# Kernel optimization log

Hardware: AMD Instinct MI355X
Metric: run time of the kernel (lower is better)

Reference implementation:

```python
import jax, jax.numpy as jnp
import numpy as np
import math

DIM = 384; HEADS = 12; HD = 32; L_REL = 4; L_STD = 12; MLP_H = 4 * DIM
B = 8; N = 256
N_REL = 1
TIME_SCALE = 30000.0 / 500 * 0.3
SCALE = HD ** -0.5
NEG = -1e9  # finite stand-in for -inf padding mask (identical softmax result, safe grads)


def _ln(x, g, b):
    m = x.mean(-1, keepdims=True)
    v = ((x - m) ** 2).mean(-1, keepdims=True)
    return (x - m) / jnp.sqrt(v + 1e-5) * g + b


def _sin_emb(x, dim):
    half = dim // 2
    freq = jnp.exp(jnp.arange(half, dtype=x.dtype) * (-math.log(10000.0) / half))
    e = x[..., None] * freq
    return jnp.concatenate([jnp.sin(e), jnp.cos(e)], -1)


def _rel_bias(x0, w1d, b1d, wp, bp):
    pos = x0[..., :3]
    t = x0[..., 3:4]
    dpos = pos[:, :, None] - pos[:, None, :]                 # [B,N,N,3]
    dt = t[:, :, None] - t[:, None, :] * TIME_SCALE          # [B,N,N,1] (scale on 2nd term, as in torch)
    dpos2 = dpos ** 2
    dt2 = dt ** 2
    ds2 = dpos2.sum(-1) - dt2[..., 0]
    d = jnp.sign(ds2) * jnp.sqrt(jnp.abs(ds2))
    f = jnp.concatenate([dpos, dt, dpos2, dt2], -1)          # [B,N,N,8]
    d = d + (f @ w1d.T + b1d)[..., 0]
    emb = _sin_emb(1024.0 * jnp.clip(d, -4.0, 4.0), HD)      # [B,N,N,HD]
    return emb @ wp.T + bp


def _mask_bias(mask):
    mn = jnp.minimum(mask[:, None, :], mask[:, :, None])
    mx = jnp.maximum(mask[:, None, :], mask[:, :, None])
    return jnp.where(mx < 0, 0.0, mn)                        # [B,N,N]


def _attn(xq, xkv, wq, wk, wv, wo, bo, rel, mbias):
    Bq, Nq, _ = xq.shape
    q = (xq @ wq.T).reshape(Bq, Nq, HEADS, HD).transpose(0, 2, 1, 3) * SCALE
    k = (xkv @ wk.T).reshape(Bq, Nq, HEADS, HD).transpose(0, 2, 1, 3)
    v = (xkv @ wv.T).reshape(Bq, Nq, HEADS, HD).transpose(0, 2, 1, 3)
    a = jnp.einsum('bhic,bhjc->bhij', q, k)
    if rel is not None:
        a = a + jnp.einsum('bhic,bijc->bhij', q, rel)
    if mbias is not None:
        a = a + mbias[:, None]
    a = jax.nn.softmax(a, axis=-1)
    o = jnp.einsum('bhij,bhjc->bihc', a, v)
    if rel is not None:
        o = o + jnp.einsum('bhij,bijc->bihc', a, rel)
    return o.reshape(Bq, Nq, HEADS * HD) @ wo.T + bo


def _mlp(x, w1, b1, w2, b2):
    return jax.nn.gelu(x @ w1.T + b1, approximate=False) @ w2.T + b2


def setup_inputs() -> dict:
    key = jax.random.key(0)
    ks = iter(jax.random.split(key, 64))
    f = lambda shape: jax.random.normal(next(ks), shape, jnp.float32) * 0.02
    inp = {}
    inp['x'] = jax.random.normal(next(ks), (B, N, DIM), jnp.float32)
    inp['x0'] = jax.random.normal(next(ks), (B, N, 4), jnp.float32)
    lengths = jax.random.randint(next(ks), (B,), N // 2, N + 1)
    inp['mask'] = jnp.where(jnp.arange(N)[None, :] < lengths[:, None], 0.0, NEG).astype(jnp.float32)
    inp['rp_w1d'] = f((1, 8)); inp['rp_b1d'] = jnp.zeros((1,), jnp.float32)
    inp['rp_wp'] = f((HD, HD)); inp['rp_bp'] = jnp.zeros((HD,), jnp.float32)
    for p, L in (('sw', L_REL), ('bl', L_STD)):
        inp[p + '_ln1_g'] = jnp.ones((L, DIM), jnp.float32); inp[p + '_ln1_b'] = jnp.zeros((L, DIM), jnp.float32)
        inp[p + '_ln2_g'] = jnp.ones((L, DIM), jnp.float32); inp[p + '_ln2_b'] = jnp.zeros((L, DIM), jnp.float32)
        inp[p + '_wq'] = f((L, DIM, DIM)); inp[p + '_wk'] = f((L, DIM, DIM)); inp[p + '_wv'] = f((L, DIM, DIM))
        inp[p + '_wo'] = f((L, DIM, DIM)); inp[p + '_bo'] = jnp.zeros((L, DIM), jnp.float32)
        inp[p + '_w1'] = f((L, MLP_H, DIM)); inp[p + '_b1'] = jnp.zeros((L, MLP_H), jnp.float32)
        inp[p + '_w2'] = f((L, DIM, MLP_H)); inp[p + '_b2'] = jnp.zeros((L, DIM), jnp.float32)
    inp['bl_g1'] = jnp.ones((L_STD, DIM), jnp.float32)   # init_values=1
    inp['bl_g2'] = jnp.ones((L_STD, DIM), jnp.float32)
    inp['cls_w'] = f((DIM,))
    inp['out_w'] = f((3, DIM)); inp['out_b'] = jnp.zeros((3,), jnp.float32)
    return inp


def reference(x, x0, mask, rp_w1d, rp_b1d, rp_wp, rp_bp,
              sw_ln1_g, sw_ln1_b, sw_ln2_g, sw_ln2_b, sw_wq, sw_wk, sw_wv, sw_wo, sw_bo,
              sw_w1, sw_b1, sw_w2, sw_b2,
              bl_ln1_g, bl_ln1_b, bl_ln2_g, bl_ln2_b, bl_wq, bl_wk, bl_wv, bl_wo, bl_bo,
              bl_w1, bl_b1, bl_w2, bl_b2, bl_g1, bl_g2, cls_w, out_w, out_b):
    rel = _rel_bias(x0, rp_w1d, rp_b1d, rp_wp, rp_bp)
    mbias = _mask_bias(mask)
    for i in range(L_REL):
        r = rel if i < N_REL else None
        xn = _ln(x, sw_ln1_g[i], sw_ln1_b[i])
        x = x + _attn(xn, xn, sw_wq[i], sw_wk[i], sw_wv[i], sw_wo[i], sw_bo[i], r, mbias)
        x = x + _mlp(_ln(x, sw_ln2_g[i], sw_ln2_b[i]), sw_w1[i], sw_b1[i], sw_w2[i], sw_b2[i])
    # prepend cls token; it is always valid
    cls = jnp.broadcast_to(cls_w[None, None, :], (x.shape[0], 1, DIM))
    x = jnp.concatenate([cls, x], axis=1)
    mask2 = jnp.concatenate([jnp.zeros((x.shape[0], 1), mask.dtype), mask], axis=1)
    mbias2 = _mask_bias(mask2)
    for i in range(L_STD):
        xn = _ln(x, bl_ln1_g[i], bl_ln1_b[i])
        x = x + bl_g1[i] * _attn(xn, xn, bl_wq[i], bl_wk[i], bl_wv[i], bl_wo[i], bl_bo[i], None, mbias2)
        x = x + bl_g2[i] * _mlp(_ln(x, bl_ln2_g[i], bl_ln2_b[i]), bl_w1[i], bl_b1[i], bl_w2[i], bl_b2[i])
    return x[:, 0] @ out_w.T + out_b   # [B, 3]
```

## Files before the change

kernel.cpp:

```cpp
#include <hip/hip_runtime.h>
#include <hip/hip_bf16.h>
#include <math.h>

#define DIM 384
#define HEADS 12
#define HD 32
#define MLP_H 1536
#define BATCH 8
#define N1 256
#define N2 257
#define QP 1152
#define SCALE 0.17677669529663687f
#define TIME_SCALE 18.0f

typedef __attribute__((ext_vector_type(8))) short frag8;
typedef __attribute__((ext_vector_type(4))) float f32x4;

__device__ inline short f2bf(float x) {
    __hip_bfloat16 h = __float2bfloat16(x);
    short s;
    __builtin_memcpy(&s, &h, 2);
    return s;
}
__device__ inline float bf2f(short s) {
    unsigned u = ((unsigned)(unsigned short)s) << 16;
    float f;
    __builtin_memcpy(&f, &u, 4);
    return f;
}

__global__ __launch_bounds__(256) void conv_kernel(
        const float* __restrict__ in, short* __restrict__ out, int n) {
    int i = (blockIdx.x * 256 + threadIdx.x) * 4;
    if (i >= n) return;
    float4 v = *(const float4*)(in + i);
    out[i]     = f2bf(v.x);
    out[i + 1] = f2bf(v.y);
    out[i + 2] = f2bf(v.z);
    out[i + 3] = f2bf(v.w);
}

__global__ __launch_bounds__(256) void conv_qkv_kernel(
        const float* __restrict__ wq, const float* __restrict__ wk,
        const float* __restrict__ wv, short* __restrict__ out, int L) {
    size_t idx = ((size_t)blockIdx.x * 256 + threadIdx.x) * 4;
    size_t total = (size_t)L * QP * DIM;
    if (idx >= total) return;
    size_t k = idx % DIM;
    size_t row = idx / DIM;
    size_t r = row % QP;
    size_t l = row / QP;
    int which = (int)(r / DIM);
    int rr = (int)(r % DIM);
    const float* src = ((which == 0) ? wq : (which == 1) ? wk : wv)
                     + (l * DIM + rr) * DIM + k;
    float4 v = *(const float4*)src;
    out[idx]     = f2bf(v.x);
    out[idx + 1] = f2bf(v.y);
    out[idx + 2] = f2bf(v.z);
    out[idx + 3] = f2bf(v.w);
}

__global__ __launch_bounds__(256) void rel_kernel(
        const float* __restrict__ x0, const float* __restrict__ w1d,
        const float* __restrict__ b1d, const float* __restrict__ wp,
        const float* __restrict__ bp, short* __restrict__ rel) {
    __shared__ float swp[HD * HD];
    __shared__ float sbp[HD];
    __shared__ float sw1[8];
    __shared__ float sb1;
    __shared__ float sfreq[16];
    int tid = threadIdx.x;
    for (int i = tid; i < HD * HD; i += 256) swp[i] = wp[i];
    if (tid < HD) sbp[tid] = bp[tid];
    if (tid < 8) sw1[tid] = w1d[tid];
    if (tid == 0) sb1 = b1d[0];
    if (tid < 16) sfreq[tid] = expf(-(float)tid * 0.5756462732485114f);
    __syncthreads();

    int gid = blockIdx.x * 256 + tid;
    int j  = gid & (N1 - 1);
    int bi = gid >> 8;
    int i  = bi & (N1 - 1);
    int b  = bi >> 8;

    const float* pi = x0 + (size_t)(b * N1 + i) * 4;
    const float* pj = x0 + (size_t)(b * N1 + j) * 4;
    float dx = pi[0] - pj[0], dy = pi[1] - pj[1], dz = pi[2] - pj[2];
    float dt = pi[3] - pj[3] * TIME_SCALE;
    float dx2 = dx * dx, dy2 = dy * dy, dz2 = dz * dz, dt2 = dt * dt;
    float ds2 = dx2 + dy2 + dz2 - dt2;
    float d = copysignf(sqrtf(fabsf(ds2)), ds2);
    d += dx * sw1[0] + dy * sw1[1] + dz * sw1[2] + dt * sw1[3]
       + dx2 * sw1[4] + dy2 * sw1[5] + dz2 * sw1[6] + dt2 * sw1[7] + sb1;
    d = fminf(fmaxf(d, -4.f), 4.f) * 1024.f;

    float emb[32];
    #pragma unroll
    for (int k = 0; k < 16; k++) {
        float s, c;
        sincosf(d * sfreq[k], &s, &c);
        emb[k] = s; emb[16 + k] = c;
    }
    short* out = rel + (size_t)gid * HD;
    #pragma unroll 4
    for (int c = 0; c < HD; c++) {
        float a = sbp[c];
        #pragma unroll
        for (int k = 0; k < 32; k++) a += emb[k] * swp[c * 32 + k];
        out[c] = f2bf(a);
    }
}

__global__ __launch_bounds__(256) void rel_score_kernel(
        const short* __restrict__ qkv, const short* __restrict__ relb,
        short* __restrict__ rs) {
    int tid = threadIdx.x;
    int w = tid >> 6, lane = tid & 63;
    int n = lane & 15, quad = lane >> 4;
    int i = blockIdx.x * 4 + w;
    int b = blockIdx.y;

    const frag8 fz = {0, 0, 0, 0, 0, 0, 0, 0};
    frag8 qa = fz;
    if (n < HEADS)
        qa = *(const frag8*)(qkv + ((size_t)(b * N1) + i) * QP + n * HD + quad * 8);

    const short* relrow = relb + (((size_t)(b * N1) + i) * N1) * HD;
    const f32x4 z = {0.f, 0.f, 0.f, 0.f};

    #pragma unroll 4
    for (int jt = 0; jt < 16; jt++) {
        frag8 rb = *(const frag8*)(relrow + (size_t)(jt * 16 + n) * HD + quad * 8);
        f32x4 s = __builtin_amdgcn_mfma_f32_16x16x32_bf16(qa, rb, z, 0, 0, 0);
        #pragma unroll
        for (int r = 0; r < 4; r++) {
            int h = quad * 4 + r;
            if (h < HEADS)
                rs[((size_t)(b * HEADS + h) * N1 + i) * N1 + jt * 16 + n] =
                    f2bf(s[r] * SCALE);
        }
    }
}

__global__ __launch_bounds__(128) void ln_kernel(
        const float* __restrict__ x, const float* __restrict__ g,
        const float* __restrict__ b, short* __restrict__ y) {
    int r = blockIdx.x;
    int t = threadIdx.x;
    const float* xr = x + (size_t)r * DIM;
    float v0 = xr[t], v1 = xr[t + 128], v2 = xr[t + 256];
    __shared__ float redm[2], redv[2];
    float s = v0 + v1 + v2;
    for (int o = 32; o; o >>= 1) s += __shfl_down(s, o, 64);
    int lane = t & 63, wid = t >> 6;
    if (!lane) redm[wid] = s;
    __syncthreads();
    float mean = (redm[0] + redm[1]) * (1.f / DIM);
    float d0 = v0 - mean, d1 = v1 - mean, d2 = v2 - mean;
    float s2 = d0 * d0 + d1 * d1 + d2 * d2;
    for (int o = 32; o; o >>= 1) s2 += __shfl_down(s2, o, 64);
    if (!lane) redv[wid] = s2;
    __syncthreads();
    float var = (redv[0] + redv[1]) * (1.f / DIM);
    float rs = rsqrtf(var + 1e-5f);
    short* yr = y + (size_t)r * DIM;
    yr[t]       = f2bf(d0 * rs * g[t]       + b[t]);
    yr[t + 128] = f2bf(d1 * rs * g[t + 128] + b[t + 128]);
    yr[t + 256] = f2bf(d2 * rs * g[t + 256] + b[t + 256]);
}

__global__ __launch_bounds__(512) void gemm_bf16_kernel(
        const short* __restrict__ A, const short* __restrict__ W,
        const float* __restrict__ bias, const float* __restrict__ resid,
        const float* __restrict__ gvec, float* __restrict__ Cf,
        short* __restrict__ Cb, int M, int Np, int K, int mode) {
    __shared__ short As2[2][2][4][64][8];
    __shared__ short Bs2[2][2][4][64][8];
    int tid = threadIdx.x;
    int w = tid >> 6, lane = tid & 63;
    int nlo = lane & 15, quad = lane >> 4;
    int g = w >> 2, wl = w & 3;
    int wm = wl >> 1, wn = wl & 1;
    int n0 = blockIdx.x * 64, m0 = blockIdx.y * 64;

    f32x4 acc00 = {0.f, 0.f, 0.f, 0.f}, acc01 = {0.f, 0.f, 0.f, 0.f};
    f32x4 acc10 = {0.f, 0.f, 0.f, 0.f}, acc11 = {0.f, 0.f, 0.f, 0.f};

    int oct16 = tid & 15, rbase = tid >> 4;
    int kh_s = oct16 >> 3, oo = oct16 & 7, ks_s = oo >> 2, q_s = oo & 3;
    const frag8 fz = {0, 0, 0, 0, 0, 0, 0, 0};
    frag8 pa0 = fz, pa1 = fz, pb0, pb1;

    {
        int gm0 = m0 + rbase, gm1 = m0 + rbase + 32;
        if (gm0 < M) pa0 = *(const frag8*)(A + (size_t)gm0 * K + oct16 * 8);
        if (gm1 < M) pa1 = *(const frag8*)(A + (size_t)gm1 * K + oct16 * 8);
        pb0 = *(const frag8*)(W + (size_t)(n0 + rbase) * K + oct16 * 8);
        pb1 = *(const frag8*)(W + (size_t)(n0 + rbase + 32) * K + oct16 * 8);
    }

    for (int k0 = 0; k0 < K; k0 += 128) {
        *(frag8*)&As2[kh_s][ks_s][q_s][rbase][0]      = pa0;
        *(frag8*)&As2[kh_s][ks_s][q_s][rbase + 32][0] = pa1;
        *(frag8*)&Bs2[kh_s][ks_s][q_s][rbase][0]      = pb0;
        *(frag8*)&Bs2[kh_s][ks_s][q_s][rbase + 32][0] = pb1;
        __syncthreads();
        int kn = k0 + 128;
        if (kn < K) {
            int gm0 = m0 + rbase, gm1 = m0 + rbase + 32;
            pa0 = fz; pa1 = fz;
            if (gm0 < M) pa0 = *(const frag8*)(A + (size_t)gm0 * K + kn + oct16 * 8);
            if (gm1 < M) pa1 = *(const frag8*)(A + (size_t)gm1 * K + kn + oct16 * 8);
            pb0 = *(const frag8*)(W + (size_t)(n0 + rbase) * K + kn + oct16 * 8);
            pb1 = *(const frag8*)(W + (size_t)(n0 + rbase + 32) * K + kn + oct16 * 8);
        }
        #pragma unroll
        for (int ks = 0; ks < 2; ks++) {
            frag8 a0 = *(const frag8*)&As2[g][ks][quad][wm * 32 + nlo][0];
            frag8 a1 = *(const frag8*)&As2[g][ks][quad][wm * 32 + 16 + nlo][0];
            frag8 b0 = *(const frag8*)&Bs2[g][ks][quad][wn * 32 + nlo][0];
            frag8 b1 = *(const frag8*)&Bs2[g][ks][quad][wn * 32 + 16 + nlo][0];
            acc00 = __builtin_amdgcn_mfma_f32_16x16x32_bf16(a0, b0, acc00, 0, 0, 0);
            acc01 = __builtin_amdgcn_mfma_f32_16x16x32_bf16(a0, b1, acc01, 0, 0, 0);
            acc10 = __builtin_amdgcn_mfma_f32_16x16x32_bf16(a1, b0, acc10, 0, 0, 0);
            acc11 = __builtin_amdgcn_mfma_f32_16x16x32_bf16(a1, b1, acc11, 0, 0, 0);
        }
        __syncthreads();
    }

    f32x4* red4 = (f32x4*)&As2[0][0][0][0][0];
    int roff = wl * 64 + lane;
    if (g == 1) {
        red4[roff]       = acc00;
        red4[256 + roff] = acc01;
        red4[512 + roff] = acc10;
        red4[768 + roff] = acc11;
    }
    __syncthreads();
    if (g == 1) return;
    {
        f32x4 t0 = red4[roff], t1 = red4[256 + roff];
        f32x4 t2 = red4[512 + roff], t3 = red4[768 + roff];
        #pragma unroll
        for (int r = 0; r < 4; r++) {
            acc00[r] += t0[r]; acc01[r] += t1[r];
            acc10[r] += t2[r]; acc11[r] += t3[r];
        }
    }

    #pragma unroll
    for (int mi = 0; mi < 2; mi++) {
        #pragma unroll
        for (int nf = 0; nf < 2; nf++) {
            f32x4 av = (mi == 0) ? ((nf == 0) ? acc00 : acc01)
                                 : ((nf == 0) ? acc10 : acc11);
            int col = n0 + wn * 32 + nf * 16 + nlo;
            float bcol = (mode >= 1) ? bias[col] : 0.f;
            float gs = 1.f;
            if (mode == 2 && gvec) gs = gvec[col];
            #pragma unroll
            for (int r = 0; r < 4; r++) {
                int row = m0 + wm * 32 + mi * 16 + quad * 4 + r;
                if (row >= M) continue;
                float v = av[r] + bcol;
                if (mode == 1) v = 0.5f * v * (1.f + erff(v * 0.70710678118654752f));
                if (mode == 2) {
                    Cf[(size_t)row * Np + col] = resid[(size_t)row * Np + col] + gs * v;
                } else {
                    Cb[(size_t)row * Np + col] = f2bf(v);
                }
            }
        }
    }
}

__global__ __launch_bounds__(256) void attn_mfma_kernel(
        const short* __restrict__ qkv, const float* __restrict__ maskv,
        short* __restrict__ ob, int Nseq) {
    __shared__ short kf[18][64][8];
    __shared__ short vf[9][2][64][8];
    __shared__ short pbuf[4][16][40];
    __shared__ float ms[320];

    int tid = threadIdx.x;
    int w = tid >> 6, lane = tid & 63;
    int n = lane & 15, quad = lane >> 4;
    int qg = blockIdx.x, h = blockIdx.y, b = blockIdx.z;
    size_t rowB = (size_t)(b * Nseq);

    for (int j = tid; j < 320; j += 256)
        ms[j] = (j < Nseq) ? maskv[b * Nseq + j] : 0.f;

    {
        int c0 = (tid & 3) * 8;
        for (int j = tid >> 2; j < 288; j += 64) {
            frag8 kk = {0, 0, 0, 0, 0, 0, 0, 0};
            frag8 vv = {0, 0, 0, 0, 0, 0, 0, 0};
            if (j < Nseq) {
                const short* base = qkv + (rowB + j) * QP + h * HD + c0;
                kk = *(const frag8*)(base + 384);
                vv = *(const frag8*)(base + 768);
            }
            *(frag8*)&kf[j >> 4][(c0 >> 3) * 16 + (j & 15)][0] = kk;
            #pragma unroll
            for (int e = 0; e < 8; e++) {
                int c = c0 + e;
                vf[j >> 5][c >> 4][((j & 31) >> 3) * 16 + (c & 15)][j & 7] = vv[e];
            }
        }
    }

    int i0 = qg * 64 + w * 16;
    frag8 qa = {0, 0, 0, 0, 0, 0, 0, 0};
    {
        int i = i0 + n;
        if (i < Nseq) qa = *(const frag8*)(qkv + (rowB + i) * QP + h * HD + quad * 8);
    }
    __syncthreads();

    float msq[4];
    #pragma unroll
    for (int r = 0; r < 4; r++) msq[r] = ms[i0 + quad * 4 + r];

    float mrow[4], lsum[4];
    #pragma unroll
    for (int r = 0; r < 4; r++) { mrow[r] = -3.0e38f; lsum[r] = 0.f; }
    f32x4 oacc0 = {0.f, 0.f, 0.f, 0.f}, oacc1 = {0.f, 0.f, 0.f, 0.f};

    for (int jb = 0; jb < 9; jb++) {
        frag8 kb0 = *(const frag8*)&kf[2 * jb][lane][0];
        frag8 kb1 = *(const frag8*)&kf[2 * jb + 1][lane][0];
        f32x4 z = {0.f, 0.f, 0.f, 0.f};
        f32x4 s0 = __builtin_amdgcn_mfma_f32_16x16x32_bf16(qa, kb0, z, 0, 0, 0);
        f32x4 s1 = __builtin_amdgcn_mfma_f32_16x16x32_bf16(qa, kb1, z, 0, 0, 0);

        int j0 = jb * 32 + n;
        int j1 = j0 + 16;
        float mj0 = ms[j0], mj1 = ms[j1];
        float pad0 = (j0 < Nseq) ? 0.f : -1e9f;
        float pad1 = (j1 < Nseq) ? 0.f : -1e9f;

        #pragma unroll
        for (int r = 0; r < 4; r++) {
            float mi = msq[r];
            float b0 = ((fmaxf(mi, mj0) < 0.f) ? 0.f : fminf(mi, mj0)) + pad0;
            float b1 = ((fmaxf(mi, mj1) < 0.f) ? 0.f : fminf(mi, mj1)) + pad1;
            float v0 = s0[r] * SCALE + b0;
            float v1 = s1[r] * SCALE + b1;
            float rm = fmaxf(v0, v1);
            rm = fmaxf(rm, __shfl_xor(rm, 1));
            rm = fmaxf(rm, __shfl_xor(rm, 2));
            rm = fmaxf(rm, __shfl_xor(rm, 4));
            rm = fmaxf(rm, __shfl_xor(rm, 8));
            float mn = fmaxf(mrow[r], rm);
            float alpha = __expf(mrow[r] - mn);
            mrow[r] = mn;
            float p0 = __expf(v0 - mn);
            float p1 = __expf(v1 - mn);
            float ps = p0 + p1;
            ps += __shfl_xor(ps, 1);
            ps += __shfl_xor(ps, 2);
            ps += __shfl_xor(ps, 4);
            ps += __shfl_xor(ps, 8);
            lsum[r] = lsum[r] * alpha + ps;
            oacc0[r] *= alpha;
            oacc1[r] *= alpha;
            pbuf[w][quad * 4 + r][n]      = f2bf(p0);
            pbuf[w][quad * 4 + r][n + 16] = f2bf(p1);
        }
        __syncthreads();
        frag8 pa = *(const frag8*)&pbuf[w][n][quad * 8];
        frag8 vb0 = *(const frag8*)&vf[jb][0][lane][0];
        frag8 vb1 = *(const frag8*)&vf[jb][1][lane][0];
        oacc0 = __builtin_amdgcn_mfma_f32_16x16x32_bf16(pa, vb0, oacc0, 0, 0, 0);
        oacc1 = __builtin_amdgcn_mfma_f32_16x16x32_bf16(pa, vb1, oacc1, 0, 0, 0);
        __syncthreads();
    }

    #pragma unroll
    for (int r = 0; r < 4; r++) {
        int i = i0 + quad * 4 + r;
        if (i < Nseq) {
            float invl = 1.f / lsum[r];
            ob[(rowB + i) * DIM + h * HD + n]      = f2bf(oacc0[r] * invl);
            ob[(rowB + i) * DIM + h * HD + 16 + n] = f2bf(oacc1[r] * invl);
        }
    }
}

__global__ __launch_bounds__(128) void attn_rel_mfma_kernel(
        const short* __restrict__ qkv, const short* __restrict__ relb,
        const short* __restrict__ rs, const float* __restrict__ maskv,
        short* __restrict__ ob) {
    const int Nseq = N1;
    __shared__ short kf[16][64][8];
    __shared__ short vf[8][2][64][8];
    __shared__ short pbuf[2][16][40];
    __shared__ float orel[2][16][33];
    __shared__ float alphas[2][16];
    __shared__ float ms[256];

    int tid = threadIdx.x;
    int w = tid >> 6, lane = tid & 63;
    int n = lane & 15, quad = lane >> 4;
    int qg = blockIdx.x, h = blockIdx.y, b = blockIdx.z;
    size_t rowB = (size_t)(b * Nseq);

    for (int jj = tid; jj < 256; jj += 128) ms[jj] = maskv[b * Nseq + jj];

    {
        int c0 = (tid & 3) * 8;
        for (int j = tid >> 2; j < 256; j += 32) {
            const short* base = qkv + (rowB + j) * QP + h * HD + c0;
            frag8 kk = *(const frag8*)(base + 384);
            frag8 vv = *(const frag8*)(base + 768);
            *(frag8*)&kf[j >> 4][(c0 >> 3) * 16 + (j & 15)][0] = kk;
            #pragma unroll
            for (int e = 0; e < 8; e++) {
                int c = c0 + e;
                vf[j >> 5][c >> 4][((j & 31) >> 3) * 16 + (c & 15)][j & 7] = vv[e];
            }
        }
    }

    int i0 = qg * 32 + w * 16;
    frag8 qa = *(const frag8*)(qkv + (rowB + i0 + n) * QP + h * HD + quad * 8);
    __syncthreads();

    float msq[4];
    const short* rsp[4];
    #pragma unroll
    for (int r = 0; r < 4; r++) {
        msq[r] = ms[i0 + quad * 4 + r];
        rsp[r] = rs + ((size_t)(b * HEADS + h) * N1 + (i0 + quad * 4 + r)) * N1;
    }

    float mrow[4], lsum[4];
    #pragma unroll
    for (int r = 0; r < 4; r++) { mrow[r] = -3.0e38f; lsum[r] = 0.f; }
    f32x4 oacc0 = {0.f, 0.f, 0.f, 0.f}, oacc1 = {0.f, 0.f, 0.f, 0.f};
    float arel[8];
    #pragma unroll
    for (int e = 0; e < 8; e++) arel[e] = 0.f;

    int il = lane & 15, oct = lane >> 4;
    const short* relrow = relb + (((size_t)b * N1 + (i0 + il)) * N1) * HD + oct * 8;

    for (int jb = 0; jb < 8; jb++) {
        frag8 kb0 = *(const frag8*)&kf[2 * jb][lane][0];
        frag8 kb1 = *(const frag8*)&kf[2 * jb + 1][lane][0];
        f32x4 z = {0.f, 0.f, 0.f, 0.f};
        f32x4 s0 = __builtin_amdgcn_mfma_f32_16x16x32_bf16(qa, kb0, z, 0, 0, 0);
        f32x4 s1 = __builtin_amdgcn_mfma_f32_16x16x32_bf16(qa, kb1, z, 0, 0, 0);

        int j0 = jb * 32 + n;
        int j1 = j0 + 16;
        float mj0 = ms[j0], mj1 = ms[j1];

        #pragma unroll
        for (int r = 0; r < 4; r++) {
            float d0 = bf2f(rsp[r][j0]);
            float d1 = bf2f(rsp[r][j1]);
            float mi = msq[r];
            float b0 = (fmaxf(mi, mj0) < 0.f) ? 0.f : fminf(mi, mj0);
            float b1 = (fmaxf(mi, mj1) < 0.f) ? 0.f : fminf(mi, mj1);
            float v0 = s0[r] * SCALE + d0 + b0;
            float v1 = s1[r] * SCALE + d1 + b1;
            float rm = fmaxf(v0, v1);
            rm = fmaxf(rm, __shfl_xor(rm, 1));
            rm = fmaxf(rm, __shfl_xor(rm, 2));
            rm = fmaxf(rm, __shfl_xor(rm, 4));
            rm = fmaxf(rm, __shfl_xor(rm, 8));
            float mn = fmaxf(mrow[r], rm);
            float alpha = __expf(mrow[r] - mn);
            mrow[r] = mn;
            float p0 = __expf(v0 - mn);
            float p1 = __expf(v1 - mn);
            float ps = p0 + p1;
            ps += __shfl_xor(ps, 1);
            ps += __shfl_xor(ps, 2);
            ps += __shfl_xor(ps, 4);
            ps += __shfl_xor(ps, 8);
            lsum[r] = lsum[r] * alpha + ps;
            oacc0[r] *= alpha;
            oacc1[r] *= alpha;
            pbuf[w][quad * 4 + r][n]      = f2bf(p0);
            pbuf[w][quad * 4 + r][n + 16] = f2bf(p1);
            if (n == 0) alphas[w][quad * 4 + r] = alpha;
        }
        __syncthreads();
        {
            float al = alphas[w][il];
            #pragma unroll
            for (int e = 0; e < 8; e++) arel[e] *= al;
            const short* rb2 = relrow + (size_t)(jb * 32) * HD;
            #pragma unroll 8
            for (int jj = 0; jj < 32; jj++) {
                float p = bf2f(pbuf[w][il][jj]);
                frag8 rv = *(const frag8*)(rb2 + (size_t)jj * HD);
                #pragma unroll
                for (int e = 0; e < 8; e++) arel[e] += p * bf2f(rv[e]);
            }
        }
        frag8 pa = *(const frag8*)&pbuf[w][n][quad * 8];
        frag8 vb0 = *(const frag8*)&vf[jb][0][lane][0];
        frag8 vb1 = *(const frag8*)&vf[jb][1][lane][0];
        oacc0 = __builtin_amdgcn_mfma_f32_16x16x32_bf16(pa, vb0, oacc0, 0, 0, 0);
        oacc1 = __builtin_amdgcn_mfma_f32_16x16x32_bf16(pa, vb1, oacc1, 0, 0, 0);
        __syncthreads();
    }

    #pragma unroll
    for (int e = 0; e < 8; e++) orel[w][il][oct * 8 + e] = arel[e];
    __syncthreads();

    #pragma unroll
    for (int r = 0; r < 4; r++) {
        int i = i0 + quad * 4 + r;
        float invl = 1.f / lsum[r];
        float o0 = (oacc0[r] + orel[w][quad * 4 + r][n])      * invl;
        float o1 = (oacc1[r] + orel[w][quad * 4 + r][16 + n]) * invl;
        ob[(rowB + i) * DIM + h * HD + n]      = f2bf(o0);
        ob[(rowB + i) * DIM + h * HD + 16 + n] = f2bf(o1);
    }
}

__global__ __launch_bounds__(256) void concat_kernel(
        const float* __restrict__ xa, const float* __restrict__ clsw,
        const float* __restrict__ mask, float* __restrict__ xb,
        float* __restrict__ m2) {
    int idx = blockIdx.x * 256 + threadIdx.x;
    const int total = BATCH * N2 * DIM;
    if (idx < total) {
        int c = idx % DIM;
        int tokb = idx / DIM;
        int p = tokb % N2, b = tokb / N2;
        xb[idx] = (p == 0) ? clsw[c] : xa[((size_t)(b * N1) + p - 1) * DIM + c];
    }
    if (idx < BATCH * N2) {
        int p = idx % N2, b = idx / N2;
        m2[idx] = (p == 0) ? 0.f : mask[b * N1 + p - 1];
    }
}

__global__ __launch_bounds__(64) void head_kernel(
        const float* __restrict__ xb, const float* __restrict__ ow,
        const float* __restrict__ obv, float* __restrict__ out) {
    int blk = blockIdx.x;
    int b = blk / 3, o = blk % 3;
    int lane = threadIdx.x;
    const float* xr = xb + (size_t)(b * N2) * DIM;
    const float* wr = ow + o * DIM;
    float s = 0.f;
    for (int c = lane; c < DIM; c += 64) s += xr[c] * wr[c];
    for (int off = 32; off; off >>= 1) s += __shfl_down(s, off, 64);
    if (!lane) out[blk] = s + obv[o];
}

extern "C" void kernel_launch(void* const* d_in, const int* in_sizes, int n_in,
                              void* d_out, int out_size, void* d_ws, size_t ws_size,
                              hipStream_t stream) {
    (void)in_sizes; (void)n_in; (void)out_size; (void)ws_size;
    const float* X       = (const float*)d_in[0];
    const float* X0      = (const float*)d_in[1];
    const float* MSK     = (const float*)d_in[2];
    const float* RW1     = (const float*)d_in[3];
    const float* RB1     = (const float*)d_in[4];
    const float* RWP     = (const float*)d_in[5];
    const float* RBP     = (const float*)d_in[6];
    const float* SW_LN1G = (const float*)d_in[7];
    const float* SW_LN1B = (const float*)d_in[8];
    const float* SW_LN2G = (const float*)d_in[9];
    const float* SW_LN2B = (const float*)d_in[10];
    const float* SW_WQ   = (const float*)d_in[11];
    const float* SW_WK   = (const float*)d_in[12];
    const float* SW_WV   = (const float*)d_in[13];
    const float* SW_WO   = (const float*)d_in[14];
    const float* SW_BO   = (const float*)d_in[15];
    const float* SW_W1   = (const float*)d_in[16];
    const float* SW_B1   = (const float*)d_in[17];
    const float* SW_W2   = (const float*)d_in[18];
    const float* SW_B2   = (const float*)d_in[19];
    const float* BL_LN1G = (const float*)d_in[20];
    const float* BL_LN1B = (const float*)d_in[21];
    const float* BL_LN2G = (const float*)d_in[22];
    const float* BL_LN2B = (const float*)d_in[23];
    const float* BL_WQ   = (const float*)d_in[24];
    const float* BL_WK   = (const float*)d_in[25];
    const float* BL_WV   = (const float*)d_in[26];
    const float* BL_WO   = (const float*)d_in[27];
    const float* BL_BO   = (const float*)d_in[28];
    const float* BL_W1   = (const float*)d_in[29];
    const float* BL_B1   = (const float*)d_in[30];
    const float* BL_W2   = (const float*)d_in[31];
    const float* BL_B2   = (const float*)d_in[32];
    const float* BL_G1   = (const float*)d_in[33];
    const float* BL_G2   = (const float*)d_in[34];
    const float* CLSW    = (const float*)d_in[35];
    const float* OUTW    = (const float*)d_in[36];
    const float* OUTB    = (const float*)d_in[37];

    const int T1 = BATCH * N1;
    const int T2 = BATCH * N2;
    const size_t RELSZ = (size_t)BATCH * N1 * N1 * HD;

    short* rel = (short*)d_ws;
    float* xa  = (float*)(rel + RELSZ);
    float* xb  = xa + (size_t)T1 * DIM;
    float* m2  = xb + (size_t)T2 * DIM;
    short* sbase = (short*)(m2 + 2064);
    short* xn   = sbase;
    short* qkv  = xn  + (size_t)T2 * DIM;
    short* ab   = qkv + (size_t)T2 * QP;
    short* hb   = ab  + (size_t)T2 * DIM;
    short* cw_qkv_sw = hb + (size_t)T2 * MLP_H;
    short* cw_qkv_bl = cw_qkv_sw + (size_t)4  * QP * DIM;
    short* cw_wo_sw  = cw_qkv_bl + (size_t)12 * QP * DIM;
    short* cw_wo_bl  = cw_wo_sw  + (size_t)4  * DIM * DIM;
    short* cw_w1_sw  = cw_wo_bl  + (size_t)12 * DIM * DIM;
    short* cw_w1_bl  = cw_w1_sw  + (size_t)4  * MLP_H * DIM;
    short* cw_w2_sw  = cw_w1_bl  + (size_t)12 * MLP_H * DIM;
    short* cw_w2_bl  = cw_w2_sw  + (size_t)4  * DIM * MLP_H;
    short* rs_buf    = cw_w2_bl  + (size_t)12 * DIM * MLP_H;

    conv_qkv_kernel<<<(4 * QP * DIM / 4 + 255) / 256, 256, 0, stream>>>(SW_WQ, SW_WK, SW_WV, cw_qkv_sw, 4);
    conv_qkv_kernel<<<(12 * QP * DIM / 4 + 255) / 256, 256, 0, stream>>>(BL_WQ, BL_WK, BL_WV, cw_qkv_bl, 12);
    conv_kernel<<<(4 * DIM * DIM / 4 + 255) / 256, 256, 0, stream>>>(SW_WO, cw_wo_sw, 4 * DIM * DIM);
    conv_kernel<<<(12 * DIM * DIM / 4 + 255) / 256, 256, 0, stream>>>(BL_WO, cw_wo_bl, 12 * DIM * DIM);
    conv_kernel<<<(4 * MLP_H * DIM / 4 + 255) / 256, 256, 0, stream>>>(SW_W1, cw_w1_sw, 4 * MLP_H * DIM);
    conv_kernel<<<(12 * MLP_H * DIM / 4 + 255) / 256, 256, 0, stream>>>(BL_W1, cw_w1_bl, 12 * MLP_H * DIM);
    conv_kernel<<<(4 * DIM * MLP_H / 4 + 255) / 256, 256, 0, stream>>>(SW_W2, cw_w2_sw, 4 * DIM * MLP_H);
    conv_kernel<<<(12 * DIM * MLP_H / 4 + 255) / 256, 256, 0, stream>>>(BL_W2, cw_w2_bl, 12 * DIM * MLP_H);

    rel_kernel<<<BATCH * N1 * N1 / 256, 256, 0, stream>>>(X0, RW1, RB1, RWP, RBP, rel);
    hipMemcpyAsync(xa, X, sizeof(float) * T1 * DIM, hipMemcpyDeviceToDevice, stream);

    dim3 gQ1(QP / 64, T1 / 64);
    dim3 gP1(DIM / 64, T1 / 64);
    dim3 gM1(MLP_H / 64, T1 / 64);
    dim3 gF1(4, HEADS, BATCH);
    dim3 gRel(8, HEADS, BATCH);
    for (int l = 0; l < 4; l++) {
        const short* wqkv = cw_qkv_sw + (size_t)l * QP * DIM;
        const short* wo = cw_wo_sw + (size_t)l * DIM * DIM;
        const short* w1 = cw_w1_sw + (size_t)l * MLP_H * DIM;
        const short* w2 = cw_w2_sw + (size_t)l * DIM * MLP_H;
        const float* bo = SW_BO + (size_t)l * DIM;
        const float* b1 = SW_B1 + (size_t)l * MLP_H;
        const float* b2 = SW_B2 + (size_t)l * DIM;

        ln_kernel<<<T1, 128, 0, stream>>>(xa, SW_LN1G + l * DIM, SW_LN1B + l * DIM, xn);
        gemm_bf16_kernel<<<gQ1, 512, 0, stream>>>(xn, wqkv, nullptr, nullptr, nullptr,
                                                  nullptr, qkv, T1, QP, DIM, 0);
        if (l == 0) {
            rel_score_kernel<<<dim3(N1 / 4, BATCH), 256, 0, stream>>>(qkv, rel, rs_buf);
            attn_rel_mfma_kernel<<<gRel, 128, 0, stream>>>(qkv, rel, rs_buf, MSK, ab);
        } else {
            attn_mfma_kernel<<<gF1, 256, 0, stream>>>(qkv, MSK, ab, N1);
        }
        gemm_bf16_kernel<<<gP1, 512, 0, stream>>>(ab, wo, bo, xa, nullptr,
                                                  xa, nullptr, T1, DIM, DIM, 2);
        ln_kernel<<<T1, 128, 0, stream>>>(xa, SW_LN2G + l * DIM, SW_LN2B + l * DIM, xn);
        gemm_bf16_kernel<<<gM1, 512, 0, stream>>>(xn, w1, b1, nullptr, nullptr,
                                                  nullptr, hb, T1, MLP_H, DIM, 1);
        gemm_bf16_kernel<<<gP1, 512, 0, stream>>>(hb, w2, b2, xa, nullptr,
                                                  xa, nullptr, T1, DIM, MLP_H, 2);
    }

    concat_kernel<<<(BATCH * N2 * DIM + 255) / 256, 256, 0, stream>>>(xa, CLSW, MSK, xb, m2);

    int MB2 = (T2 + 63) / 64;
    dim3 gQ2(QP / 64, MB2);
    dim3 gP2(DIM / 64, MB2);
    dim3 gM2(MLP_H / 64, MB2);
    dim3 gF2(5, HEADS, BATCH);
    for (int l = 0; l < 12; l++) {
        const short* wqkv = cw_qkv_bl + (size_t)l * QP * DIM;
        const short* wo = cw_wo_bl + (size_t)l * DIM * DIM;
        const short* w1 = cw_w1_bl + (size_t)l * MLP_H * DIM;
        const short* w2 = cw_w2_bl + (size_t)l * DIM * MLP_H;
        const float* bo = BL_BO + (size_t)l * DIM;
        const float* b1 = BL_B1 + (size_t)l * MLP_H;
        const float* b2 = BL_B2 + (size_t)l * DIM;
        const float* g1 = BL_G1 + (size_t)l * DIM;
        const float* g2 = BL_G2 + (size_t)l * DIM;

        ln_kernel<<<T2, 128, 0, stream>>>(xb, BL_LN1G + l * DIM, BL_LN1B + l * DIM, xn);
        gemm_bf16_kernel<<<gQ2, 512, 0, stream>>>(xn, wqkv, nullptr, nullptr, nullptr,
                                                  nullptr, qkv, T2, QP, DIM, 0);
        attn_mfma_kernel<<<gF2, 256, 0, stream>>>(qkv, m2, ab, N2);
        gemm_bf16_kernel<<<gP2, 512, 0, stream>>>(ab, wo, bo, xb, g1,
                                                  xb, nullptr, T2, DIM, DIM, 2);
        ln_kernel<<<T2, 128, 0, stream>>>(xb, BL_LN2G + l * DIM, BL_LN2B + l * DIM, xn);
        gemm_bf16_kernel<<<gM2, 512, 0, stream>>>(xn, w1, b1, nullptr, nullptr,
                                                  nullptr, hb, T2, MLP_H, DIM, 1);
        gemm_bf16_kernel<<<gP2, 512, 0, stream>>>(hb, w2, b2, xb, g2,
                                                  xb, nullptr, T2, DIM, MLP_H, 2);
    }

    head_kernel<<<BATCH * 3, 64, 0, stream>>>(xb, OUTW, OUTB, (float*)d_out);
}
```

Baseline: 1.811 ms.

## Split relative-position PV into separate MFMA kernel and drop attention barriers

The rel-attention kernel now computes an exact two-pass softmax held in registers and writes the normalized probabilities back into the score buffer. A new rel_pv_kernel then multiplies those probabilities by the relative tensor with MFMA and adds the main attention output, replacing the scalar per-lane rel accumulation loop. Both attention kernels double-buffer the per-wave probability tile and remove the __syncthreads inside the key loop, since each wave only touches its own slice. This trades an extra kernel launch and fp32 round trip through global memory, plus higher register pressure, for less scalar work and fewer barriers.

```diff
diff --git a/kernel.cpp b/kernel.cpp
--- a/kernel.cpp
+++ b/kernel.cpp
@@ -139,6 +139,57 @@
             if (h < HEADS)
                 rs[((size_t)(b * HEADS + h) * N1 + i) * N1 + jt * 16 + n] =
                     f2bf(s[r] * SCALE);
+        }
+    }
+}
+
+__global__ __launch_bounds__(256) void rel_pv_kernel(
+        const short* __restrict__ pglob, const short* __restrict__ relb,
+        const float* __restrict__ omain, short* __restrict__ ob) {
+    __shared__ short vt[4][2][2][64][8];
+    int tid = threadIdx.x;
+    int w = tid >> 6, lane = tid & 63;
+    int n = lane & 15, quad = lane >> 4;
+    int i = blockIdx.x * 4 + w;
+    int b = blockIdx.y;
+    size_t rowB = (size_t)(b * N1);
+
+    const frag8 fz = {0, 0, 0, 0, 0, 0, 0, 0};
+    f32x4 oa0 = {0.f, 0.f, 0.f, 0.f}, oa1 = {0.f, 0.f, 0.f, 0.f};
+    const short* relrow = relb + ((rowB + i) * (size_t)N1) * HD;
+    const short* prow = pglob + ((size_t)(b * HEADS + (n < HEADS ? n : 0)) * N1 + i) * N1;
+    bool hval = (n < HEADS);
+
+    int jr = lane & 31;
+    int cb = (lane >> 5) * 16;
+
+    #pragma unroll 2
+    for (int kk = 0; kk < 8; kk++) {
+        int par = kk & 1;
+        const short* rr = relrow + (size_t)(kk * 32 + jr) * HD + cb;
+        frag8 rv0 = *(const frag8*)rr;
+        frag8 rv1 = *(const frag8*)(rr + 8);
+        #pragma unroll
+        for (int e = 0; e < 8; e++) {
+            int c0 = cb + e, c1 = cb + 8 + e;
+            vt[w][par][c0 >> 4][(jr >> 3) * 16 + (c0 & 15)][jr & 7] = rv0[e];
+            vt[w][par][c1 >> 4][(jr >> 3) * 16 + (c1 & 15)][jr & 7] = rv1[e];
+        }
+        frag8 pa = fz;
+        if (hval) pa = *(const frag8*)(prow + kk * 32 + quad * 8);
+        frag8 b0 = *(const frag8*)&vt[w][par][0][lane][0];
+        frag8 b1 = *(const frag8*)&vt[w][par][1][lane][0];
+        oa0 = __builtin_amdgcn_mfma_f32_16x16x32_bf16(pa, b0, oa0, 0, 0, 0);
+        oa1 = __builtin_amdgcn_mfma_f32_16x16x32_bf16(pa, b1, oa1, 0, 0, 0);
+    }
+
+    #pragma unroll
+    for (int r = 0; r < 4; r++) {
+        int h = quad * 4 + r;
+        if (h < HEADS) {
+            size_t o0 = (rowB + i) * DIM + h * HD + n;
+            ob[o0]      = f2bf(omain[o0]      + oa0[r]);
+            ob[o0 + 16] = f2bf(omain[o0 + 16] + oa1[r]);
         }
     }
 }
@@ -280,7 +331,7 @@
         short* __restrict__ ob, int Nseq) {
     __shared__ short kf[18][64][8];
     __shared__ short vf[9][2][64][8];
-    __shared__ short pbuf[4][16][40];
+    __shared__ short pbuf[4][2][16][40];
     __shared__ float ms[320];
 
     int tid = threadIdx.x;
@@ -329,6 +380,7 @@
     f32x4 oacc0 = {0.f, 0.f, 0.f, 0.f}, oacc1 = {0.f, 0.f, 0.f, 0.f};
 
     for (int jb = 0; jb < 9; jb++) {
+        int par = jb & 1;
         frag8 kb0 = *(const frag8*)&kf[2 * jb][lane][0];
         frag8 kb1 = *(const frag8*)&kf[2 * jb + 1][lane][0];
         f32x4 z = {0.f, 0.f, 0.f, 0.f};
@@ -366,16 +418,14 @@
             lsum[r] = lsum[r] * alpha + ps;
             oacc0[r] *= alpha;
             oacc1[r] *= alpha;
-            pbuf[w][quad * 4 + r][n]      = f2bf(p0);
-            pbuf[w][quad * 4 + r][n + 16] = f2bf(p1);
-        }
-        __syncthreads();
-        frag8 pa = *(const frag8*)&pbuf[w][n][quad * 8];
+            pbuf[w][par][quad * 4 + r][n]      = f2bf(p0);
+            pbuf[w][par][quad * 4 + r][n + 16] = f2bf(p1);
+        }
+        frag8 pa = *(const frag8*)&pbuf[w][par][n][quad * 8];
         frag8 vb0 = *(const frag8*)&vf[jb][0][lane][0];
         frag8 vb1 = *(const frag8*)&vf[jb][1][lane][0];
         oacc0 = __builtin_amdgcn_mfma_f32_16x16x32_bf16(pa, vb0, oacc0, 0, 0, 0);
         oacc1 = __builtin_amdgcn_mfma_f32_16x16x32_bf16(pa, vb1, oacc1, 0, 0, 0);
-        __syncthreads();
     }
 
     #pragma unroll
@@ -390,15 +440,12 @@
 }
 
 __global__ __launch_bounds__(128) void attn_rel_mfma_kernel(
-        const short* __restrict__ qkv, const short* __restrict__ relb,
-        const short* __restrict__ rs, const float* __restrict__ maskv,
-        short* __restrict__ ob) {
+        const short* __restrict__ qkv, short* __restrict__ rs,
+        const float* __restrict__ maskv, float* __restrict__ omain) {
     const int Nseq = N1;
     __shared__ short kf[16][64][8];
     __shared__ short vf[8][2][64][8];
-    __shared__ short pbuf[2][16][40];
-    __shared__ float orel[2][16][33];
-    __shared__ float alphas[2][16];
+    __shared__ short pbuf[2][2][16][40];
     __shared__ float ms[256];
 
     int tid = threadIdx.x;
@@ -429,35 +476,28 @@
     __syncthreads();
 
     float msq[4];
-    const short* rsp[4];
+    short* rsp[4];
     #pragma unroll
     for (int r = 0; r < 4; r++) {
         msq[r] = ms[i0 + quad * 4 + r];
         rsp[r] = rs + ((size_t)(b * HEADS + h) * N1 + (i0 + quad * 4 + r)) * N1;
     }
 
-    float mrow[4], lsum[4];
-    #pragma unroll
-    for (int r = 0; r < 4; r++) { mrow[r] = -3.0e38f; lsum[r] = 0.f; }
-    f32x4 oacc0 = {0.f, 0.f, 0.f, 0.f}, oacc1 = {0.f, 0.f, 0.f, 0.f};
-    float arel[8];
-    #pragma unroll
-    for (int e = 0; e < 8; e++) arel[e] = 0.f;
-
-    int il = lane & 15, oct = lane >> 4;
-    const short* relrow = relb + (((size_t)b * N1 + (i0 + il)) * N1) * HD + oct * 8;
-
+    float sv0[32], sv1[32];
+    float rmax[4];
+    #pragma unroll
+    for (int r = 0; r < 4; r++) rmax[r] = -3.0e38f;
+
+    #pragma unroll
     for (int jb = 0; jb < 8; jb++) {
         frag8 kb0 = *(const frag8*)&kf[2 * jb][lane][0];
         frag8 kb1 = *(const frag8*)&kf[2 * jb + 1][lane][0];
         f32x4 z = {0.f, 0.f, 0.f, 0.f};
         f32x4 s0 = __builtin_amdgcn_mfma_f32_16x16x32_bf16(qa, kb0, z, 0, 0, 0);
         f32x4 s1 = __builtin_amdgcn_mfma_f32_16x16x32_bf16(qa, kb1, z, 0, 0, 0);
-
         int j0 = jb * 32 + n;
         int j1 = j0 + 16;
         float mj0 = ms[j0], mj1 = ms[j1];
-
         #pragma unroll
         for (int r = 0; r < 4; r++) {
             float d0 = bf2f(rsp[r][j0]);
@@ -467,62 +507,69 @@
             float b1 = (fmaxf(mi, mj1) < 0.f) ? 0.f : fminf(mi, mj1);
             float v0 = s0[r] * SCALE + d0 + b0;
             float v1 = s1[r] * SCALE + d1 + b1;
-            float rm = fmaxf(v0, v1);
-            rm = fmaxf(rm, __shfl_xor(rm, 1));
-            rm = fmaxf(rm, __shfl_xor(rm, 2));
-            rm = fmaxf(rm, __shfl_xor(rm, 4));
-            rm = fmaxf(rm, __shfl_xor(rm, 8));
-            float mn = fmaxf(mrow[r], rm);
-            float alpha = __expf(mrow[r] - mn);
-            mrow[r] = mn;
-            float p0 = __expf(v0 - mn);
-            float p1 = __expf(v1 - mn);
-            float ps = p0 + p1;
-            ps += __shfl_xor(ps, 1);
-            ps += __shfl_xor(ps, 2);
-            ps += __shfl_xor(ps, 4);
-            ps += __shfl_xor(ps, 8);
-            lsum[r] = lsum[r] * alpha + ps;
-            oacc0[r] *= alpha;
-            oacc1[r] *= alpha;
-            pbuf[w][quad * 4 + r][n]      = f2bf(p0);
-            pbuf[w][quad * 4 + r][n + 16] = f2bf(p1);
-            if (n == 0) alphas[w][quad * 4 + r] = alpha;
-        }
-        __syncthreads();
-        {
-            float al = alphas[w][il];
-            #pragma unroll
-            for (int e = 0; e < 8; e++) arel[e] *= al;
-            const short* rb2 = relrow + (size_t)(jb * 32) * HD;
-            #pragma unroll 8
-            for (int jj = 0; jj < 32; jj++) {
-                float p = bf2f(pbuf[w][il][jj]);
-                frag8 rv = *(const frag8*)(rb2 + (size_t)jj * HD);
-                #pragma unroll
-                for (int e = 0; e < 8; e++) arel[e] += p * bf2f(rv[e]);
-            }
-        }
-        frag8 pa = *(const frag8*)&pbuf[w][n][quad * 8];
+            sv0[jb * 4 + r] = v0;
+            sv1[jb * 4 + r] = v1;
+            rmax[r] = fmaxf(rmax[r], fmaxf(v0, v1));
+        }
+    }
+    #pragma unroll
+    for (int r = 0; r < 4; r++) {
+        float rm = rmax[r];
+        rm = fmaxf(rm, __shfl_xor(rm, 1));
+        rm = fmaxf(rm, __shfl_xor(rm, 2));
+        rm = fmaxf(rm, __shfl_xor(rm, 4));
+        rm = fmaxf(rm, __shfl_xor(rm, 8));
+        rmax[r] = rm;
+    }
+
+    float lsum[4] = {0.f, 0.f, 0.f, 0.f};
+    #pragma unroll
+    for (int jb = 0; jb < 8; jb++) {
+        #pragma unroll
+        for (int r = 0; r < 4; r++) {
+            float p0 = __expf(sv0[jb * 4 + r] - rmax[r]);
+            float p1 = __expf(sv1[jb * 4 + r] - rmax[r]);
+            sv0[jb * 4 + r] = p0;
+            sv1[jb * 4 + r] = p1;
+            lsum[r] += p0 + p1;
+        }
+    }
+    float invl[4];
+    #pragma unroll
+    for (int r = 0; r < 4; r++) {
+        float ls = lsum[r];
+        ls += __shfl_xor(ls, 1);
+        ls += __shfl_xor(ls, 2);
+        ls += __shfl_xor(ls, 4);
+        ls += __shfl_xor(ls, 8);
+        invl[r] = 1.f / ls;
+    }
+
+    f32x4 oacc0 = {0.f, 0.f, 0.f, 0.f}, oacc1 = {0.f, 0.f, 0.f, 0.f};
+    #pragma unroll
+    for (int jb = 0; jb < 8; jb++) {
+        int par = jb & 1;
+        #pragma unroll
+        for (int r = 0; r < 4; r++) {
+            short h0 = f2bf(sv0[jb * 4 + r] * invl[r]);
+            short h1 = f2bf(sv1[jb * 4 + r] * invl[r]);
+            pbuf[w][par][quad * 4 + r][n]      = h0;
+            pbuf[w][par][quad * 4 + r][n + 16] = h1;
+            rsp[r][jb * 32 + n]      = h0;
+            rsp[r][jb * 32 + n + 16] = h1;
+        }
+        frag8 pa = *(const frag8*)&pbuf[w][par][n][quad * 8];
         frag8 vb0 = *(const frag8*)&vf[jb][0][lane][0];
         frag8 vb1 = *(const frag8*)&vf[jb][1][lane][0];
         oacc0 = __builtin_amdgcn_mfma_f32_16x16x32_bf16(pa, vb0, oacc0, 0, 0, 0);
         oacc1 = __builtin_amdgcn_mfma_f32_16x16x32_bf16(pa, vb1, oacc1, 0, 0, 0);
-        __syncthreads();
-    }
-
-    #pragma unroll
-    for (int e = 0; e < 8; e++) orel[w][il][oct * 8 + e] = arel[e];
-    __syncthreads();
+    }
 
     #pragma unroll
     for (int r = 0; r < 4; r++) {
         int i = i0 + quad * 4 + r;
-        float invl = 1.f / lsum[r];
-        float o0 = (oacc0[r] + orel[w][quad * 4 + r][n])      * invl;
-        float o1 = (oacc1[r] + orel[w][quad * 4 + r][16 + n]) * invl;
-        ob[(rowB + i) * DIM + h * HD + n]      = f2bf(o0);
-        ob[(rowB + i) * DIM + h * HD + 16 + n] = f2bf(o1);
+        omain[(rowB + i) * DIM + h * HD + n]      = oacc0[r];
+        omain[(rowB + i) * DIM + h * HD + 16 + n] = oacc1[r];
     }
 }
 
@@ -623,6 +670,7 @@
     short* cw_w2_sw  = cw_w1_bl  + (size_t)12 * MLP_H * DIM;
     short* cw_w2_bl  = cw_w2_sw  + (size_t)4  * DIM * MLP_H;
     short* rs_buf    = cw_w2_bl  + (size_t)12 * DIM * MLP_H;
+    float* omain     = (float*)hb;
 
     conv_qkv_kernel<<<(4 * QP * DIM / 4 + 255) / 256, 256, 0, stream>>>(SW_WQ, SW_WK, SW_WV, cw_qkv_sw, 4);
     conv_qkv_kernel<<<(12 * QP * DIM / 4 + 255) / 256, 256, 0, stream>>>(BL_WQ, BL_WK, BL_WV, cw_qkv_bl, 12);
@@ -655,7 +703,8 @@
                                                   nullptr, qkv, T1, QP, DIM, 0);
         if (l == 0) {
             rel_score_kernel<<<dim3(N1 / 4, BATCH), 256, 0, stream>>>(qkv, rel, rs_buf);
-            attn_rel_mfma_kernel<<<gRel, 128, 0, stream>>>(qkv, rel, rs_buf, MSK, ab);
+            attn_rel_mfma_kernel<<<gRel, 128, 0, stream>>>(qkv, rs_buf, MSK, omain);
+            rel_pv_kernel<<<dim3(N1 / 4, BATCH), 256, 0, stream>>>(rs_buf, rel, omain, ab);
         } else {
             attn_mfma_kernel<<<gF1, 256, 0, stream>>>(qkv, MSK, ab, N1);
         }
```

New measurement: 1.755 ms. 1.03x faster.
